# Kernel optimization log

Measured on AMD Instinct MI355X. Metric: run time of the kernel, lower is better.

Reference implementation:

```python
import jax, jax.numpy as jnp
import numpy as np

N_NODES, SEQ_LEN, IN_CH, HID, OUT_CH, N_EDGES = 10000, 12, 16, 64, 1, 160000


def setup_inputs() -> dict:
    key = jax.random.key(0)
    ks = jax.random.split(key, 16)
    s = 1.0 / np.sqrt(HID)
    u = lambda k, shape: jax.random.uniform(k, shape, jnp.float32, -s, s)
    return {
        "x_seq": jax.random.normal(ks[0], (1, SEQ_LEN, N_NODES, IN_CH), jnp.float32),
        "edge_index": jax.random.randint(ks[1], (2, N_EDGES), 0, N_NODES, jnp.int32),
        "gcn_w": jax.random.normal(ks[2], (IN_CH, HID), jnp.float32) / np.sqrt(IN_CH),
        "gcn_b": jnp.zeros((HID,), jnp.float32),
        "w_ih0": u(ks[3], (3 * HID, HID)),
        "w_hh0": u(ks[4], (3 * HID, HID)),
        "b_ih0": u(ks[5], (3 * HID,)),
        "b_hh0": u(ks[6], (3 * HID,)),
        "w_ih1": u(ks[7], (3 * HID, HID)),
        "w_hh1": u(ks[8], (3 * HID, HID)),
        "b_ih1": u(ks[9], (3 * HID,)),
        "b_hh1": u(ks[10], (3 * HID,)),
        "attn_w": u(ks[11], (HID, 1)),
        "attn_b": u(ks[12], (1,)),
        "fc_w": u(ks[13], (HID, OUT_CH)),
        "fc_b": u(ks[14], (OUT_CH,)),
    }


def _gcn_all_t(x_ntf, edge_index, w, b):
    # x_ntf: (N, T, F). Symmetric-normalized GCNConv with self loops (PyG default),
    # applied to every timestep at once (edge structure is static).
    n = x_ntf.shape[0]
    loop = jnp.arange(n, dtype=edge_index.dtype)
    src = jnp.concatenate([edge_index[0], loop])
    dst = jnp.concatenate([edge_index[1], loop])
    deg = jax.ops.segment_sum(jnp.ones_like(src, dtype=x_ntf.dtype), dst, num_segments=n)
    dis = jax.lax.rsqrt(deg)  # deg >= 1 thanks to self loops
    norm = dis[src] * dis[dst]  # (E+N,)
    msg = x_ntf[src] * norm[:, None, None]  # (E+N, T, F)
    agg = jax.ops.segment_sum(msg, dst, num_segments=n)  # (N, T, F)
    return agg @ w + b  # (N, T, H)


def _gru_layer(x, w_ih, w_hh, b_ih, b_hh):
    # x: (B, T, Hin) batch_first; PyTorch GRU cell equations, h0 = 0.
    bsz, _, _ = x.shape
    h_dim = w_hh.shape[1]
    xi = x @ w_ih.T + b_ih  # (B, T, 3H), precomputed input projections

    def step(h, xt):
        gh = h @ w_hh.T + b_hh
        ir, iz, in_ = jnp.split(xt, 3, axis=-1)
        hr, hz, hn = jnp.split(gh, 3, axis=-1)
        r = jax.nn.sigmoid(ir + hr)
        z = jax.nn.sigmoid(iz + hz)
        n = jnp.tanh(in_ + r * hn)
        h_new = (1.0 - z) * n + z * h
        return h_new, h_new

    h0 = jnp.zeros((bsz, h_dim), x.dtype)
    _, hs = jax.lax.scan(step, h0, jnp.swapaxes(xi, 0, 1))  # (T, B, H)
    return jnp.swapaxes(hs, 0, 1)


def reference(x_seq, edge_index, gcn_w, gcn_b, w_ih0, w_hh0, b_ih0, b_hh0,
              w_ih1, w_hh1, b_ih1, b_hh1, attn_w, attn_b, fc_w, fc_b):
    batch, seq_len, num_nodes, _ = x_seq.shape  # batch == 1 (see notes)
    # (B, T, N, F) -> (N, T, F)
    x_ntf = jnp.swapaxes(x_seq[0], 0, 1)
    gcn_out = jax.nn.relu(_gcn_all_t(x_ntf, edge_index, gcn_w, gcn_b))  # (N, T, H)
    # gru_input: (B*N, T, H); dropout between GRU layers disabled (inference)
    h1 = _gru_layer(gcn_out, w_ih0, w_hh0, b_ih0, b_hh0)
    gru_out = _gru_layer(h1, w_ih1, w_hh1, b_ih1, b_hh1)  # (N, T, H)
    attn_scores = jax.nn.softmax(gru_out @ attn_w + attn_b, axis=1)  # (N, T, 1)
    context = jnp.sum(attn_scores * gru_out, axis=1)  # (N, H)
    residual = (context @ fc_w + fc_b).reshape(batch, num_nodes, -1)
    last_known = x_seq[:, -1, :, 0][..., None]  # (B, N, 1)
    return last_known + residual
```

## Files before the change

### kernel.cpp

```cpp
#include <hip/hip_runtime.h>
#include <hip/hip_bf16.h>
#include <hip/hip_fp16.h>

#define N_NODES 10000
#define SEQ_T 12
#define IN_CH 16
#define HID 64
#define N_EDGES 160000
#define CAP 96
#define PB 0xAAAAAAAAu

typedef __attribute__((ext_vector_type(8))) short short8;
typedef __attribute__((ext_vector_type(4))) float floatx4;

__device__ __forceinline__ float frcp(float x){ return __builtin_amdgcn_rcpf(x); }
__device__ __forceinline__ float sigmf(float x){ return frcp(1.0f + __expf(-x)); }
__device__ __forceinline__ float tanh_fast(float x){ return 1.0f - 2.0f * frcp(1.0f + __expf(2.0f * x)); }
__device__ __forceinline__ unsigned short f2bf(float f){
  union { float f; unsigned int u; } c; c.f = f;
  unsigned int u = c.u;
  return (unsigned short)((u + 0x7FFFu + ((u >> 16) & 1u)) >> 16);
}
__device__ __forceinline__ unsigned short f2h(float f){
  _Float16 h = (_Float16)f; unsigned short u; __builtin_memcpy(&u, &h, 2); return u;
}
__device__ __forceinline__ unsigned int cvt_pk_bf16(float a, float b){
  unsigned int r;
  asm("v_cvt_pk_bf16_f32 %0, %1, %2" : "=v"(r) : "v"(a), "v"(b));
  return r;
}


__global__ void k_fill(const int* __restrict__ ei, unsigned int* __restrict__ cnt,
                       int* __restrict__ csr,
                       const float* __restrict__ wih0, const float* __restrict__ whh0,
                       const float* __restrict__ wih1, const float* __restrict__ whh1,
                       unsigned short* __restrict__ wF,
                       const float* __restrict__ x, unsigned short* __restrict__ xT){
  int i = blockIdx.x * 256 + threadIdx.x;
  if (i < 49152){
    int p = i / 12288, ii = i - p * 12288;
    const float* sp = (p & 2) ? ((p & 1) ? whh1 : wih1) : ((p & 1) ? whh0 : wih0);
    int e = ii & 7, l = (ii >> 3) & 63, jk = ii >> 9;
    int kt = jk / 12, jt = jk - kt * 12;
    int j = (l & 15) + 16 * jt;
    int k = ((l >> 4) * 8) + e + 32 * kt;
    wF[i] = f2bf(sp[j * 64 + k]);
  }
  {
    int n = i >> 4, ch = i & 15;
    const float* xp = x + (size_t)n * IN_CH + ch;
    unsigned short tmp[SEQ_T];
    #pragma unroll
    for (int t = 0; t < SEQ_T; ++t) tmp[t] = f2h(xp[(size_t)t * N_NODES * IN_CH]);
    unsigned short* dp = xT + (size_t)n * 192 + ch * 12;
    *(ushort4*)(dp)     = make_ushort4(tmp[0], tmp[1], tmp[2],  tmp[3]);
    *(ushort4*)(dp + 4) = make_ushort4(tmp[4], tmp[5], tmp[6],  tmp[7]);
    *(ushort4*)(dp + 8) = make_ushort4(tmp[8], tmp[9], tmp[10], tmp[11]);
  }
  int s = ei[i], d = ei[N_EDGES + i];
  unsigned int pos = atomicAdd(&cnt[d], 1u) - PB;
  if (pos < CAP) csr[d * CAP + pos] = s;
}

__global__ __launch_bounds__(256, 3) void k_fused(
    const float* __restrict__ x, const unsigned short* __restrict__ xT,
    const unsigned int* __restrict__ cnt, const int* __restrict__ csr,
    const float* __restrict__ gcn_w, const float* __restrict__ gcn_b,
    const unsigned short* __restrict__ wF,
    const float* __restrict__ bih0, const float* __restrict__ bhh0,
    const float* __restrict__ bih1, const float* __restrict__ bhh1,
    const float* __restrict__ attn_w, const float* __restrict__ fc_w,
    const float* __restrict__ fc_b, float* __restrict__ out){
  __shared__ union {
    struct {
      int2  eLDS[16][16];
      unsigned short smB[SEQ_T][32][8];
    } A;
    struct {
      unsigned short HL[2][16][72];
      unsigned short h1[2][16][72];
      float scdc[SEQ_T][2][16];
    } B;
  } U;
  __shared__ unsigned short gout[SEQ_T][1024];
  __shared__ float biasL[2][4][64];

  const int tid = threadIdx.x;
  const int blk = blockIdx.x;
  const int w = tid >> 6;
  const int l = tid & 63;
  const int c = l & 15;
  const int q = l >> 4;
  const int hbase = 16 * w + 4 * q;

  if (tid < 128){
    int ly = tid >> 6, hh = tid & 63;
    const float* bi = ly ? bih1 : bih0;
    const float* bh = ly ? bhh1 : bhh0;
    biasL[ly][0][hh] = bi[hh] + bh[hh];
    biasL[ly][1][hh] = bi[64 + hh] + bh[64 + hh];
    biasL[ly][2][hh] = bi[128 + hh];
    biasL[ly][3][hh] = bh[128 + hh];
  }

  short8 aW = (short8){0, 0, 0, 0, 0, 0, 0, 0};
  if (l < 32){
    int jj = (l & 15) + 16 * w;
    #pragma unroll
    for (int e = 0; e < 8; ++e){
      int k = (l >> 4) * 8 + e;
      aW[e] = (short)f2bf(gcn_w[k * HID + jj]);
    }
  }
  floatx4 gb = *(const floatx4*)(gcn_b + hbase);

  {
    const int g = tid >> 4, ch = tid & 15;
    const int dst = blk * 16 + g;
    int deg = (int)(cnt[dst] - PB);
    if (deg > CAP) deg = CAP;
    float selfdis = rsqrtf((float)deg + 1.0f);
    __half2 ah[6];
    {
      const __half2* xs = (const __half2*)(const void*)(xT + (size_t)dst * 192 + ch * 12);
      __half2 sd2 = __float2half2_rn(selfdis);
      #pragma unroll
      for (int k = 0; k < 6; ++k) ah[k] = __hmul2(sd2, xs[k]);
    }
    for (int base = 0; base < deg; base += 16){
      int ep = base + ch;
      int2 ev = make_int2(0, 0);
      if (ep < deg){
        int s = csr[dst * CAP + ep];
        ev = make_int2(s, __float_as_int(rsqrtf((float)(cnt[s] - PB) + 1.0f)));
      }
      U.A.eLDS[g][ch] = ev;
      int c2 = deg - base; if (c2 > 16) c2 = 16;
      #pragma unroll 4
      for (int j = 0; j < c2; ++j){
        int2 e2 = U.A.eLDS[g][j];
        __half2 wh = __float2half2_rn(__int_as_float(e2.y));
        const __half2* xp = (const __half2*)(const void*)(xT + (size_t)e2.x * 192 + ch * 12);
        #pragma unroll
        for (int k = 0; k < 6; ++k) ah[k] = __hfma2(wh, xp[k], ah[k]);
      }
    }
    const int lp = (ch >> 3) * 16 + g, ep2 = ch & 7;
    #pragma unroll
    for (int t = 0; t < SEQ_T; ++t){
      float f = (t & 1) ? __high2float(ah[t >> 1]) : __low2float(ah[t >> 1]);
      U.A.smB[t][lp][ep2] = f2bf(selfdis * f);
    }
    __syncthreads();
  }

  {
    const int sec = (2 * w + (q >> 1)) & 3;
    const int goff = (w >> 1) * 512 + (c + 16 * sec) * 8 + (q & 1) * 4;
    #pragma unroll
    for (int t = 0; t < SEQ_T; ++t){
      short8 xb = (short8){0, 0, 0, 0, 0, 0, 0, 0};
      if (l < 32) xb = *(const short8*)&U.A.smB[t][l][0];
      floatx4 aC = gb;
      aC = __builtin_amdgcn_mfma_f32_16x16x32_bf16(aW, xb, aC, 0, 0, 0);
      unsigned int plo = cvt_pk_bf16(fmaxf(aC[0], 0.0f), fmaxf(aC[1], 0.0f));
      unsigned int phi = cvt_pk_bf16(fmaxf(aC[2], 0.0f), fmaxf(aC[3], 0.0f));
      *(uint2*)(void*)(&gout[t][goff]) = make_uint2(plo, phi);
    }
    __syncthreads();
  }

  short8 bw0[2][3][2], bw1[2][3][2];
  #pragma unroll
  for (int g2 = 0; g2 < 2; ++g2)
    #pragma unroll
    for (int s = 0; s < 3; ++s)
      #pragma unroll
      for (int kt = 0; kt < 2; ++kt){
        int jt = w + 4 * s;
        bw0[g2][s][kt] = *(const short8*)(wF + ((((size_t)g2 * 2 + kt) * 12 + jt) * 64 + l) * 8);
        bw1[g2][s][kt] = *(const short8*)(wF + ((((size_t)(2 + g2) * 2 + kt) * 12 + jt) * 64 + l) * 8);
      }
  short8 bwA[2];
  #pragma unroll
  for (int kt = 0; kt < 2; ++kt){
    short8 v;
    #pragma unroll
    for (int e = 0; e < 8; ++e){
      int k = q * 8 + e + 32 * kt;
      float f = (c == 0) ? attn_w[k] : (c == 1) ? fc_w[k] : 0.0f;
      v[e] = (short)f2bf(f);
    }
    bwA[kt] = v;
  }

  float hp0[4] = {0.f, 0.f, 0.f, 0.f};
  float hp1[4] = {0.f, 0.f, 0.f, 0.f};
  #pragma unroll 1
  for (int i = 0; i <= SEQ_T; ++i){
    if (i < SEQ_T){
      short8 xa0 = *(const short8*)&gout[i][l * 8];
      short8 xa1 = *(const short8*)&gout[i][512 + l * 8];
      floatx4 aR  = *(const floatx4*)&biasL[0][0][hbase];
      floatx4 aZ  = *(const floatx4*)&biasL[0][1][hbase];
      floatx4 aNx = *(const floatx4*)&biasL[0][2][hbase];
      floatx4 aNh = *(const floatx4*)&biasL[0][3][hbase];
      if (i > 0){
        short8 ha0 = *(const short8*)&U.B.HL[(i - 1) & 1][c][8 * q];
        short8 ha1 = *(const short8*)&U.B.HL[(i - 1) & 1][c][8 * q + 32];
        aR  = __builtin_amdgcn_mfma_f32_16x16x32_bf16(bw0[1][0][0], ha0, aR, 0, 0, 0);
        aR  = __builtin_amdgcn_mfma_f32_16x16x32_bf16(bw0[1][0][1], ha1, aR, 0, 0, 0);
        aZ  = __builtin_amdgcn_mfma_f32_16x16x32_bf16(bw0[1][1][0], ha0, aZ, 0, 0, 0);
        aZ  = __builtin_amdgcn_mfma_f32_16x16x32_bf16(bw0[1][1][1], ha1, aZ, 0, 0, 0);
        aNh = __builtin_amdgcn_mfma_f32_16x16x32_bf16(bw0[1][2][0], ha0, aNh, 0, 0, 0);
        aNh = __builtin_amdgcn_mfma_f32_16x16x32_bf16(bw0[1][2][1], ha1, aNh, 0, 0, 0);
      }
      aR  = __builtin_amdgcn_mfma_f32_16x16x32_bf16(bw0[0][0][0], xa0, aR, 0, 0, 0);
      aR  = __builtin_amdgcn_mfma_f32_16x16x32_bf16(bw0[0][0][1], xa1, aR, 0, 0, 0);
      aZ  = __builtin_amdgcn_mfma_f32_16x16x32_bf16(bw0[0][1][0], xa0, aZ, 0, 0, 0);
      aZ  = __builtin_amdgcn_mfma_f32_16x16x32_bf16(bw0[0][1][1], xa1, aZ, 0, 0, 0);
      aNx = __builtin_amdgcn_mfma_f32_16x16x32_bf16(bw0[0][2][0], xa0, aNx, 0, 0, 0);
      aNx = __builtin_amdgcn_mfma_f32_16x16x32_bf16(bw0[0][2][1], xa1, aNx, 0, 0, 0);
      float h4[4];
      #pragma unroll
      for (int r = 0; r < 4; ++r){
        float rr = sigmf(aR[r]);
        float zz = sigmf(aZ[r]);
        float nn = tanh_fast(aNx[r] + rr * aNh[r]);
        h4[r] = nn + zz * (hp0[r] - nn);
        hp0[r] = h4[r];
      }
      *(uint2*)(void*)(&U.B.HL[i & 1][c][hbase]) =
          make_uint2(cvt_pk_bf16(h4[0], h4[1]), cvt_pk_bf16(h4[2], h4[3]));
    }
    if (i >= 1){
      int t = i - 1;
      int pr = t & 1;
      short8 xb0 = *(const short8*)&U.B.HL[pr][c][8 * q];
      short8 xb1 = *(const short8*)&U.B.HL[pr][c][8 * q + 32];
      floatx4 aR  = *(const floatx4*)&biasL[1][0][hbase];
      floatx4 aZ  = *(const floatx4*)&biasL[1][1][hbase];
      floatx4 aNx = *(const floatx4*)&biasL[1][2][hbase];
      floatx4 aNh = *(const floatx4*)&biasL[1][3][hbase];
      if (t > 0){
        short8 hb0 = *(const short8*)&U.B.h1[pr][c][8 * q];
        short8 hb1 = *(const short8*)&U.B.h1[pr][c][8 * q + 32];
        aR  = __builtin_amdgcn_mfma_f32_16x16x32_bf16(bw1[1][0][0], hb0, aR, 0, 0, 0);
        aR  = __builtin_amdgcn_mfma_f32_16x16x32_bf16(bw1[1][0][1], hb1, aR, 0, 0, 0);
        aZ  = __builtin_amdgcn_mfma_f32_16x16x32_bf16(bw1[1][1][0], hb0, aZ, 0, 0, 0);
        aZ  = __builtin_amdgcn_mfma_f32_16x16x32_bf16(bw1[1][1][1], hb1, aZ, 0, 0, 0);
        aNh = __builtin_amdgcn_mfma_f32_16x16x32_bf16(bw1[1][2][0], hb0, aNh, 0, 0, 0);
        aNh = __builtin_amdgcn_mfma_f32_16x16x32_bf16(bw1[1][2][1], hb1, aNh, 0, 0, 0);
        if (w == 0){
          floatx4 aA = (floatx4){0.f, 0.f, 0.f, 0.f};
          aA = __builtin_amdgcn_mfma_f32_16x16x32_bf16(bwA[0], hb0, aA, 0, 0, 0);
          aA = __builtin_amdgcn_mfma_f32_16x16x32_bf16(bwA[1], hb1, aA, 0, 0, 0);
          if (q == 0){
            U.B.scdc[t - 1][0][c] = aA[0];
            U.B.scdc[t - 1][1][c] = aA[1];
          }
        }
      }
      aR  = __builtin_amdgcn_mfma_f32_16x16x32_bf16(bw1[0][0][0], xb0, aR, 0, 0, 0);
      aR  = __builtin_amdgcn_mfma_f32_16x16x32_bf16(bw1[0][0][1], xb1, aR, 0, 0, 0);
      aZ  = __builtin_amdgcn_mfma_f32_16x16x32_bf16(bw1[0][1][0], xb0, aZ, 0, 0, 0);
      aZ  = __builtin_amdgcn_mfma_f32_16x16x32_bf16(bw1[0][1][1], xb1, aZ, 0, 0, 0);
      aNx = __builtin_amdgcn_mfma_f32_16x16x32_bf16(bw1[0][2][0], xb0, aNx, 0, 0, 0);
      aNx = __builtin_amdgcn_mfma_f32_16x16x32_bf16(bw1[0][2][1], xb1, aNx, 0, 0, 0);
      float h4[4];
      #pragma unroll
      for (int r = 0; r < 4; ++r){
        float rr = sigmf(aR[r]);
        float zz = sigmf(aZ[r]);
        float nn = tanh_fast(aNx[r] + rr * aNh[r]);
        h4[r] = nn + zz * (hp1[r] - nn);
        hp1[r] = h4[r];
      }
      *(uint2*)(void*)(&U.B.h1[1 - pr][c][hbase]) =
          make_uint2(cvt_pk_bf16(h4[0], h4[1]), cvt_pk_bf16(h4[2], h4[3]));
    }
    __syncthreads();
  }

  if (w == 0){
    short8 hL0 = *(const short8*)&U.B.h1[0][c][8 * q];
    short8 hL1 = *(const short8*)&U.B.h1[0][c][8 * q + 32];
    floatx4 aA = (floatx4){0.f, 0.f, 0.f, 0.f};
    aA = __builtin_amdgcn_mfma_f32_16x16x32_bf16(bwA[0], hL0, aA, 0, 0, 0);
    aA = __builtin_amdgcn_mfma_f32_16x16x32_bf16(bwA[1], hL1, aA, 0, 0, 0);
    if (q == 0){
      U.B.scdc[SEQ_T - 1][0][c] = aA[0];
      U.B.scdc[SEQ_T - 1][1][c] = aA[1];
    }
    int gn = blk * 16 + l;
    if (l < 16){
      float sc[SEQ_T], dc[SEQ_T];
      #pragma unroll
      for (int t = 0; t < SEQ_T; ++t){ sc[t] = U.B.scdc[t][0][l]; dc[t] = U.B.scdc[t][1][l]; }
      float m = sc[0];
      #pragma unroll
      for (int t = 1; t < SEQ_T; ++t) m = fmaxf(m, sc[t]);
      float den = 0.0f, num = 0.0f;
      #pragma unroll
      for (int t = 0; t < SEQ_T; ++t){
        float p = __expf(sc[t] - m);
        den += p;
        num = fmaf(p, dc[t], num);
      }
      float y = fc_b[0] + num * frcp(den);
      float last = x[((size_t)(SEQ_T - 1) * N_NODES + gn) * IN_CH];
      out[gn] = last + y;
    }
  }
}

extern "C" void kernel_launch(void* const* d_in, const int* in_sizes, int n_in,
                              void* d_out, int out_size, void* d_ws, size_t ws_size,
                              hipStream_t stream){
  const float* x = (const float*)d_in[0];
  const int* ei  = (const int*)d_in[1];
  char* ws = (char*)d_ws;
  unsigned int*   cnt = (unsigned int*)(ws);
  int*            csr = (int*)(ws + 40960);
  unsigned short* wF  = (unsigned short*)(ws + 3880960);
  unsigned short* xT  = (unsigned short*)(ws + 3979264);

  k_fill<<<625, 256, 0, stream>>>(ei, cnt, csr,
      (const float*)d_in[4], (const float*)d_in[5],
      (const float*)d_in[8], (const float*)d_in[9], wF,
      x, xT);
  k_fused<<<625, 256, 0, stream>>>(
      x, xT, cnt, csr,
      (const float*)d_in[2], (const float*)d_in[3], wF,
      (const float*)d_in[6],  (const float*)d_in[7],
      (const float*)d_in[10], (const float*)d_in[11],
      (const float*)d_in[12], (const float*)d_in[14], (const float*)d_in[15],
      (float*)d_out);
}
```

Measured before the change: 133.1 us.

## Pre-scale node features by source degree norm in separate kernel

Moves the x transpose/fp16 conversion into a new kernel that runs after the degree counts are complete and multiplies each node's features by its rsqrt degree factor. The gather loop in the fused kernel then does plain half2 adds of pre-scaled neighbours, with no per-edge lookup of cnt[s] or rsqrt and no per-edge weight in LDS. The edge staging in LDS shrinks from int2 to int. The cost is an extra kernel launch and a serial dependency on k_fill. The self-term also no longer uses the clamped degree, and fp16 accumulation of pre-scaled values may round slightly differently.

```diff
diff --git a/kernel.cpp b/kernel.cpp
--- a/kernel.cpp
+++ b/kernel.cpp
@@ -24,6 +24,9 @@
 __device__ __forceinline__ unsigned short f2h(float f){
   _Float16 h = (_Float16)f; unsigned short u; __builtin_memcpy(&u, &h, 2); return u;
 }
+__device__ __forceinline__ __half2 u32h2(unsigned int u){
+  __half2 h; __builtin_memcpy(&h, &u, 4); return h;
+}
 __device__ __forceinline__ unsigned int cvt_pk_bf16(float a, float b){
   unsigned int r;
   asm("v_cvt_pk_bf16_f32 %0, %1, %2" : "=v"(r) : "v"(a), "v"(b));
@@ -35,8 +38,7 @@
                        int* __restrict__ csr,
                        const float* __restrict__ wih0, const float* __restrict__ whh0,
                        const float* __restrict__ wih1, const float* __restrict__ whh1,
-                       unsigned short* __restrict__ wF,
-                       const float* __restrict__ x, unsigned short* __restrict__ xT){
+                       unsigned short* __restrict__ wF){
   int i = blockIdx.x * 256 + threadIdx.x;
   if (i < 49152){
     int p = i / 12288, ii = i - p * 12288;
@@ -47,20 +49,24 @@
     int k = ((l >> 4) * 8) + e + 32 * kt;
     wF[i] = f2bf(sp[j * 64 + k]);
   }
-  {
-    int n = i >> 4, ch = i & 15;
-    const float* xp = x + (size_t)n * IN_CH + ch;
-    unsigned short tmp[SEQ_T];
-    #pragma unroll
-    for (int t = 0; t < SEQ_T; ++t) tmp[t] = f2h(xp[(size_t)t * N_NODES * IN_CH]);
-    unsigned short* dp = xT + (size_t)n * 192 + ch * 12;
-    *(ushort4*)(dp)     = make_ushort4(tmp[0], tmp[1], tmp[2],  tmp[3]);
-    *(ushort4*)(dp + 4) = make_ushort4(tmp[4], tmp[5], tmp[6],  tmp[7]);
-    *(ushort4*)(dp + 8) = make_ushort4(tmp[8], tmp[9], tmp[10], tmp[11]);
-  }
   int s = ei[i], d = ei[N_EDGES + i];
   unsigned int pos = atomicAdd(&cnt[d], 1u) - PB;
   if (pos < CAP) csr[d * CAP + pos] = s;
+}
+
+__global__ void k_xt(const unsigned int* __restrict__ cnt,
+                     const float* __restrict__ x, unsigned short* __restrict__ xT){
+  int i = blockIdx.x * 256 + threadIdx.x;
+  int n = i >> 4, ch = i & 15;
+  float dis = rsqrtf((float)(cnt[n] - PB) + 1.0f);
+  const float* xp = x + (size_t)n * IN_CH + ch;
+  unsigned short tmp[SEQ_T];
+  #pragma unroll
+  for (int t = 0; t < SEQ_T; ++t) tmp[t] = f2h(dis * xp[(size_t)t * N_NODES * IN_CH]);
+  unsigned short* dp = xT + (size_t)n * 192 + ch * 12;
+  *(ushort4*)(dp)     = make_ushort4(tmp[0], tmp[1], tmp[2],  tmp[3]);
+  *(ushort4*)(dp + 4) = make_ushort4(tmp[4], tmp[5], tmp[6],  tmp[7]);
+  *(ushort4*)(dp + 8) = make_ushort4(tmp[8], tmp[9], tmp[10], tmp[11]);
 }
 
 __global__ __launch_bounds__(256, 3) void k_fused(
@@ -74,7 +80,7 @@
     const float* __restrict__ fc_b, float* __restrict__ out){
   __shared__ union {
     struct {
-      int2  eLDS[16][16];
+      int eLDSi[16][16];
       unsigned short smB[SEQ_T][32][8];
     } A;
     struct {
@@ -118,40 +124,44 @@
   {
     const int g = tid >> 4, ch = tid & 15;
     const int dst = blk * 16 + g;
-    int deg = (int)(cnt[dst] - PB);
-    if (deg > CAP) deg = CAP;
-    float selfdis = rsqrtf((float)deg + 1.0f);
-    __half2 ah[6];
+    const int degF = (int)(cnt[dst] - PB);
+    int deg = degF > CAP ? CAP : degF;
+    float selfdis = rsqrtf((float)degF + 1.0f);
+    __half2 ah0, ah1, ah2, ah3, ah4, ah5;
     {
-      const __half2* xs = (const __half2*)(const void*)(xT + (size_t)dst * 192 + ch * 12);
-      __half2 sd2 = __float2half2_rn(selfdis);
-      #pragma unroll
-      for (int k = 0; k < 6; ++k) ah[k] = __hmul2(sd2, xs[k]);
+      const uint2* xs = (const uint2*)(const void*)(xT + (size_t)dst * 192 + ch * 12);
+      uint2 a = xs[0], b = xs[1], cc = xs[2];
+      ah0 = u32h2(a.x);  ah1 = u32h2(a.y);
+      ah2 = u32h2(b.x);  ah3 = u32h2(b.y);
+      ah4 = u32h2(cc.x); ah5 = u32h2(cc.y);
     }
     for (int base = 0; base < deg; base += 16){
       int ep = base + ch;
-      int2 ev = make_int2(0, 0);
-      if (ep < deg){
-        int s = csr[dst * CAP + ep];
-        ev = make_int2(s, __float_as_int(rsqrtf((float)(cnt[s] - PB) + 1.0f)));
-      }
-      U.A.eLDS[g][ch] = ev;
+      int s = 0;
+      if (ep < deg) s = csr[dst * CAP + ep];
+      U.A.eLDSi[g][ch] = s;
       int c2 = deg - base; if (c2 > 16) c2 = 16;
       #pragma unroll 4
       for (int j = 0; j < c2; ++j){
-        int2 e2 = U.A.eLDS[g][j];
-        __half2 wh = __float2half2_rn(__int_as_float(e2.y));
-        const __half2* xp = (const __half2*)(const void*)(xT + (size_t)e2.x * 192 + ch * 12);
-        #pragma unroll
-        for (int k = 0; k < 6; ++k) ah[k] = __hfma2(wh, xp[k], ah[k]);
+        int s2 = U.A.eLDSi[g][j];
+        const uint2* xp = (const uint2*)(const void*)(xT + (size_t)s2 * 192 + ch * 12);
+        uint2 a = xp[0], b = xp[1], cc = xp[2];
+        ah0 = __hadd2(ah0, u32h2(a.x));  ah1 = __hadd2(ah1, u32h2(a.y));
+        ah2 = __hadd2(ah2, u32h2(b.x));  ah3 = __hadd2(ah3, u32h2(b.y));
+        ah4 = __hadd2(ah4, u32h2(cc.x)); ah5 = __hadd2(ah5, u32h2(cc.y));
       }
     }
     const int lp = (ch >> 3) * 16 + g, ep2 = ch & 7;
-    #pragma unroll
-    for (int t = 0; t < SEQ_T; ++t){
-      float f = (t & 1) ? __high2float(ah[t >> 1]) : __low2float(ah[t >> 1]);
-      U.A.smB[t][lp][ep2] = f2bf(selfdis * f);
-    }
+    float fv[SEQ_T];
+    fv[0]  = __low2float(ah0); fv[1]  = __high2float(ah0);
+    fv[2]  = __low2float(ah1); fv[3]  = __high2float(ah1);
+    fv[4]  = __low2float(ah2); fv[5]  = __high2float(ah2);
+    fv[6]  = __low2float(ah3); fv[7]  = __high2float(ah3);
+    fv[8]  = __low2float(ah4); fv[9]  = __high2float(ah4);
+    fv[10] = __low2float(ah5); fv[11] = __high2float(ah5);
+    #pragma unroll
+    for (int t = 0; t < SEQ_T; ++t)
+      U.A.smB[t][lp][ep2] = f2bf(selfdis * fv[t]);
     __syncthreads();
   }
 
@@ -328,8 +338,8 @@
 
   k_fill<<<625, 256, 0, stream>>>(ei, cnt, csr,
       (const float*)d_in[4], (const float*)d_in[5],
-      (const float*)d_in[8], (const float*)d_in[9], wF,
-      x, xT);
+      (const float*)d_in[8], (const float*)d_in[9], wF);
+  k_xt<<<625, 256, 0, stream>>>(cnt, x, xT);
   k_fused<<<625, 256, 0, stream>>>(
       x, xT, cnt, csr,
       (const float*)d_in[2], (const float*)d_in[3], wF,
```

Measured after the change: 137.8 us. 3.5% more time.

## Split interleaved two-layer GRU loop into sequential layer loops via LDS

Applied to the files above, without the earlier changes.

The kernel used to run GRU layer 0 and layer 1 skewed by one step in a single loop. It now runs all 12 layer-0 steps first, keeps every layer-0 hidden state in an LDS array, and then runs layer 1 as a separate loop. The two weight register sets are no longer live at the same time, which lowers register pressure. The layer-1 state and the attention scratch now reuse the LDS space of the GCN output buffer. The cost is losing the two independent dependency chains per iteration, nearly doubling the number of barriers, and a larger LDS footprint that sits close to the 3-blocks-per-CU limit. It also changes the self-loop normalization to use the uncapped degree.

```diff
diff --git a/kernel.cpp b/kernel.cpp
--- a/kernel.cpp
+++ b/kernel.cpp
@@ -23,6 +23,9 @@
 }
 __device__ __forceinline__ unsigned short f2h(float f){
   _Float16 h = (_Float16)f; unsigned short u; __builtin_memcpy(&u, &h, 2); return u;
+}
+__device__ __forceinline__ __half2 u32h2(unsigned int u){
+  __half2 h; __builtin_memcpy(&h, &u, 4); return h;
 }
 __device__ __forceinline__ unsigned int cvt_pk_bf16(float a, float b){
   unsigned int r;
@@ -77,13 +80,15 @@
       int2  eLDS[16][16];
       unsigned short smB[SEQ_T][32][8];
     } A;
+    unsigned short HL[SEQ_T][16][72];
+  } U;
+  __shared__ union {
+    unsigned short gout[SEQ_T][1024];
     struct {
-      unsigned short HL[2][16][72];
       unsigned short h1[2][16][72];
       float scdc[SEQ_T][2][16];
-    } B;
-  } U;
-  __shared__ unsigned short gout[SEQ_T][1024];
+    } C;
+  } V;
   __shared__ float biasL[2][4][64];
 
   const int tid = threadIdx.x;
@@ -118,9 +123,9 @@
   {
     const int g = tid >> 4, ch = tid & 15;
     const int dst = blk * 16 + g;
-    int deg = (int)(cnt[dst] - PB);
-    if (deg > CAP) deg = CAP;
-    float selfdis = rsqrtf((float)deg + 1.0f);
+    const int degF = (int)(cnt[dst] - PB);
+    int deg = degF > CAP ? CAP : degF;
+    float selfdis = rsqrtf((float)degF + 1.0f);
     __half2 ah[6];
     {
       const __half2* xs = (const __half2*)(const void*)(xT + (size_t)dst * 192 + ch * 12);
@@ -166,49 +171,34 @@
       aC = __builtin_amdgcn_mfma_f32_16x16x32_bf16(aW, xb, aC, 0, 0, 0);
       unsigned int plo = cvt_pk_bf16(fmaxf(aC[0], 0.0f), fmaxf(aC[1], 0.0f));
       unsigned int phi = cvt_pk_bf16(fmaxf(aC[2], 0.0f), fmaxf(aC[3], 0.0f));
-      *(uint2*)(void*)(&gout[t][goff]) = make_uint2(plo, phi);
+      *(uint2*)(void*)(&V.gout[t][goff]) = make_uint2(plo, phi);
     }
     __syncthreads();
   }
 
-  short8 bw0[2][3][2], bw1[2][3][2];
-  #pragma unroll
-  for (int g2 = 0; g2 < 2; ++g2)
-    #pragma unroll
-    for (int s = 0; s < 3; ++s)
-      #pragma unroll
-      for (int kt = 0; kt < 2; ++kt){
-        int jt = w + 4 * s;
-        bw0[g2][s][kt] = *(const short8*)(wF + ((((size_t)g2 * 2 + kt) * 12 + jt) * 64 + l) * 8);
-        bw1[g2][s][kt] = *(const short8*)(wF + ((((size_t)(2 + g2) * 2 + kt) * 12 + jt) * 64 + l) * 8);
-      }
-  short8 bwA[2];
-  #pragma unroll
-  for (int kt = 0; kt < 2; ++kt){
-    short8 v;
-    #pragma unroll
-    for (int e = 0; e < 8; ++e){
-      int k = q * 8 + e + 32 * kt;
-      float f = (c == 0) ? attn_w[k] : (c == 1) ? fc_w[k] : 0.0f;
-      v[e] = (short)f2bf(f);
-    }
-    bwA[kt] = v;
-  }
-
-  float hp0[4] = {0.f, 0.f, 0.f, 0.f};
-  float hp1[4] = {0.f, 0.f, 0.f, 0.f};
-  #pragma unroll 1
-  for (int i = 0; i <= SEQ_T; ++i){
-    if (i < SEQ_T){
-      short8 xa0 = *(const short8*)&gout[i][l * 8];
-      short8 xa1 = *(const short8*)&gout[i][512 + l * 8];
+  {
+    short8 bw0[2][3][2];
+    #pragma unroll
+    for (int g2 = 0; g2 < 2; ++g2)
+      #pragma unroll
+      for (int s = 0; s < 3; ++s)
+        #pragma unroll
+        for (int kt = 0; kt < 2; ++kt){
+          int jt = w + 4 * s;
+          bw0[g2][s][kt] = *(const short8*)(wF + ((((size_t)g2 * 2 + kt) * 12 + jt) * 64 + l) * 8);
+        }
+    float hp0[4] = {0.f, 0.f, 0.f, 0.f};
+    #pragma unroll 1
+    for (int t = 0; t < SEQ_T; ++t){
+      short8 xa0 = *(const short8*)&V.gout[t][l * 8];
+      short8 xa1 = *(const short8*)&V.gout[t][512 + l * 8];
       floatx4 aR  = *(const floatx4*)&biasL[0][0][hbase];
       floatx4 aZ  = *(const floatx4*)&biasL[0][1][hbase];
       floatx4 aNx = *(const floatx4*)&biasL[0][2][hbase];
       floatx4 aNh = *(const floatx4*)&biasL[0][3][hbase];
-      if (i > 0){
-        short8 ha0 = *(const short8*)&U.B.HL[(i - 1) & 1][c][8 * q];
-        short8 ha1 = *(const short8*)&U.B.HL[(i - 1) & 1][c][8 * q + 32];
+      if (t > 0){
+        short8 ha0 = *(const short8*)&U.HL[t - 1][c][8 * q];
+        short8 ha1 = *(const short8*)&U.HL[t - 1][c][8 * q + 32];
         aR  = __builtin_amdgcn_mfma_f32_16x16x32_bf16(bw0[1][0][0], ha0, aR, 0, 0, 0);
         aR  = __builtin_amdgcn_mfma_f32_16x16x32_bf16(bw0[1][0][1], ha1, aR, 0, 0, 0);
         aZ  = __builtin_amdgcn_mfma_f32_16x16x32_bf16(bw0[1][1][0], ha0, aZ, 0, 0, 0);
@@ -231,21 +221,48 @@
         h4[r] = nn + zz * (hp0[r] - nn);
         hp0[r] = h4[r];
       }
-      *(uint2*)(void*)(&U.B.HL[i & 1][c][hbase]) =
+      *(uint2*)(void*)(&U.HL[t][c][hbase]) =
           make_uint2(cvt_pk_bf16(h4[0], h4[1]), cvt_pk_bf16(h4[2], h4[3]));
-    }
-    if (i >= 1){
-      int t = i - 1;
+      __syncthreads();
+    }
+  }
+
+  {
+    short8 bw1[2][3][2];
+    #pragma unroll
+    for (int g2 = 0; g2 < 2; ++g2)
+      #pragma unroll
+      for (int s = 0; s < 3; ++s)
+        #pragma unroll
+        for (int kt = 0; kt < 2; ++kt){
+          int jt = w + 4 * s;
+          bw1[g2][s][kt] = *(const short8*)(wF + ((((size_t)(2 + g2) * 2 + kt) * 12 + jt) * 64 + l) * 8);
+        }
+    short8 bwA[2];
+    #pragma unroll
+    for (int kt = 0; kt < 2; ++kt){
+      short8 v;
+      #pragma unroll
+      for (int e = 0; e < 8; ++e){
+        int k = q * 8 + e + 32 * kt;
+        float f = (c == 0) ? attn_w[k] : (c == 1) ? fc_w[k] : 0.0f;
+        v[e] = (short)f2bf(f);
+      }
+      bwA[kt] = v;
+    }
+    float hp1[4] = {0.f, 0.f, 0.f, 0.f};
+    #pragma unroll 1
+    for (int t = 0; t < SEQ_T; ++t){
       int pr = t & 1;
-      short8 xb0 = *(const short8*)&U.B.HL[pr][c][8 * q];
-      short8 xb1 = *(const short8*)&U.B.HL[pr][c][8 * q + 32];
+      short8 xb0 = *(const short8*)&U.HL[t][c][8 * q];
+      short8 xb1 = *(const short8*)&U.HL[t][c][8 * q + 32];
       floatx4 aR  = *(const floatx4*)&biasL[1][0][hbase];
       floatx4 aZ  = *(const floatx4*)&biasL[1][1][hbase];
       floatx4 aNx = *(const floatx4*)&biasL[1][2][hbase];
       floatx4 aNh = *(const floatx4*)&biasL[1][3][hbase];
       if (t > 0){
-        short8 hb0 = *(const short8*)&U.B.h1[pr][c][8 * q];
-        short8 hb1 = *(const short8*)&U.B.h1[pr][c][8 * q + 32];
+        short8 hb0 = *(const short8*)&V.C.h1[pr][c][8 * q];
+        short8 hb1 = *(const short8*)&V.C.h1[pr][c][8 * q + 32];
         aR  = __builtin_amdgcn_mfma_f32_16x16x32_bf16(bw1[1][0][0], hb0, aR, 0, 0, 0);
         aR  = __builtin_amdgcn_mfma_f32_16x16x32_bf16(bw1[1][0][1], hb1, aR, 0, 0, 0);
         aZ  = __builtin_amdgcn_mfma_f32_16x16x32_bf16(bw1[1][1][0], hb0, aZ, 0, 0, 0);
@@ -257,8 +274,8 @@
           aA = __builtin_amdgcn_mfma_f32_16x16x32_bf16(bwA[0], hb0, aA, 0, 0, 0);
           aA = __builtin_amdgcn_mfma_f32_16x16x32_bf16(bwA[1], hb1, aA, 0, 0, 0);
           if (q == 0){
-            U.B.scdc[t - 1][0][c] = aA[0];
-            U.B.scdc[t - 1][1][c] = aA[1];
+            V.C.scdc[t - 1][0][c] = aA[0];
+            V.C.scdc[t - 1][1][c] = aA[1];
           }
         }
       }
@@ -277,40 +294,40 @@
         h4[r] = nn + zz * (hp1[r] - nn);
         hp1[r] = h4[r];
       }
-      *(uint2*)(void*)(&U.B.h1[1 - pr][c][hbase]) =
+      *(uint2*)(void*)(&V.C.h1[1 - pr][c][hbase]) =
           make_uint2(cvt_pk_bf16(h4[0], h4[1]), cvt_pk_bf16(h4[2], h4[3]));
-    }
-    __syncthreads();
-  }
-
-  if (w == 0){
-    short8 hL0 = *(const short8*)&U.B.h1[0][c][8 * q];
-    short8 hL1 = *(const short8*)&U.B.h1[0][c][8 * q + 32];
-    floatx4 aA = (floatx4){0.f, 0.f, 0.f, 0.f};
-    aA = __builtin_amdgcn_mfma_f32_16x16x32_bf16(bwA[0], hL0, aA, 0, 0, 0);
-    aA = __builtin_amdgcn_mfma_f32_16x16x32_bf16(bwA[1], hL1, aA, 0, 0, 0);
-    if (q == 0){
-      U.B.scdc[SEQ_T - 1][0][c] = aA[0];
-      U.B.scdc[SEQ_T - 1][1][c] = aA[1];
-    }
-    int gn = blk * 16 + l;
-    if (l < 16){
-      float sc[SEQ_T], dc[SEQ_T];
-      #pragma unroll
-      for (int t = 0; t < SEQ_T; ++t){ sc[t] = U.B.scdc[t][0][l]; dc[t] = U.B.scdc[t][1][l]; }
-      float m = sc[0];
-      #pragma unroll
-      for (int t = 1; t < SEQ_T; ++t) m = fmaxf(m, sc[t]);
-      float den = 0.0f, num = 0.0f;
-      #pragma unroll
-      for (int t = 0; t < SEQ_T; ++t){
-        float p = __expf(sc[t] - m);
-        den += p;
-        num = fmaf(p, dc[t], num);
-      }
-      float y = fc_b[0] + num * frcp(den);
-      float last = x[((size_t)(SEQ_T - 1) * N_NODES + gn) * IN_CH];
-      out[gn] = last + y;
+      __syncthreads();
+    }
+
+    if (w == 0){
+      short8 hL0 = *(const short8*)&V.C.h1[0][c][8 * q];
+      short8 hL1 = *(const short8*)&V.C.h1[0][c][8 * q + 32];
+      floatx4 aA = (floatx4){0.f, 0.f, 0.f, 0.f};
+      aA = __builtin_amdgcn_mfma_f32_16x16x32_bf16(bwA[0], hL0, aA, 0, 0, 0);
+      aA = __builtin_amdgcn_mfma_f32_16x16x32_bf16(bwA[1], hL1, aA, 0, 0, 0);
+      if (q == 0){
+        V.C.scdc[SEQ_T - 1][0][c] = aA[0];
+        V.C.scdc[SEQ_T - 1][1][c] = aA[1];
+      }
+      int gn = blk * 16 + l;
+      if (l < 16){
+        float sc[SEQ_T], dc[SEQ_T];
+        #pragma unroll
+        for (int t = 0; t < SEQ_T; ++t){ sc[t] = V.C.scdc[t][0][l]; dc[t] = V.C.scdc[t][1][l]; }
+        float m = sc[0];
+        #pragma unroll
+        for (int t = 1; t < SEQ_T; ++t) m = fmaxf(m, sc[t]);
+        float den = 0.0f, num = 0.0f;
+        #pragma unroll
+        for (int t = 0; t < SEQ_T; ++t){
+          float p = __expf(sc[t] - m);
+          den += p;
+          num = fmaf(p, dc[t], num);
+        }
+        float y = fc_b[0] + num * frcp(den);
+        float last = x[((size_t)(SEQ_T - 1) * N_NODES + gn) * IN_CH];
+        out[gn] = last + y;
+      }
     }
   }
 }
```

New measurement: 147.2 us. 1.11x slower.
